# Kernel optimization log

Hardware: AMD Instinct MI355X
Metric: run time of the kernel (lower is better)

## Reference

```python
import jax, jax.numpy as jnp
import numpy as np

# dims
B, L, D, H, HD, V, FF, NL = 1, 1024, 1024, 16, 64, 32000, 2816, 2
THETA = 500000.0
EPS = 1e-5
BOI, EOI = 31998, 31999
NEG = jnp.float32(-1e30)  # stands in for -inf in the additive mask


def setup_inputs() -> dict:
    key = jax.random.key(0)
    ks = jax.random.split(key, 12)
    tokens = jax.random.randint(ks[0], (B, L), 0, 31998)
    # inject two well-formed image spans per sequence (boi .. eoi)
    tokens = tokens.at[:, 100].set(BOI).at[:, 300].set(EOI)
    tokens = tokens.at[:, 500].set(BOI).at[:, 800].set(EOI)
    s = 0.02
    n = lambda k, shape: (jax.random.normal(k, shape, jnp.float32) * s)
    return {
        "tokens": tokens,
        "tok_emb": n(ks[1], (V, D)),
        "wq": n(ks[2], (NL, D, D)),
        "wk": n(ks[3], (NL, D, D)),
        "wv": n(ks[4], (NL, D, D)),
        "wo": n(ks[5], (NL, D, D)),
        "w1": n(ks[6], (NL, FF, D)),
        "w2": n(ks[7], (NL, D, FF)),
        "w3": n(ks[8], (NL, FF, D)),
        "attn_norm_w": jnp.ones((NL, D), jnp.float32),
        "ffn_norm_w": jnp.ones((NL, D), jnp.float32),
        "final_norm_w": jnp.ones((D,), jnp.float32),
        "w_out": n(ks[9], (V, D)),
    }


def rmsnorm(x, w):
    xf = x.astype(jnp.float32)
    y = xf * jax.lax.rsqrt(jnp.mean(xf * xf, axis=-1, keepdims=True) + EPS)
    return y.astype(x.dtype) * w


def rope_cos_sin():
    inv = 1.0 / (THETA ** (jnp.arange(0, HD, 2, dtype=jnp.float32) / HD))  # [HD/2]
    ang = jnp.arange(L, dtype=jnp.float32)[:, None] * inv[None, :]        # [L, HD/2]
    return jnp.cos(ang), jnp.sin(ang)


def apply_rope(x, cos, sin):
    # x: [B, L, H, HD]; pairs (even, odd) rotated by complex freqs_cis
    xr = x.astype(jnp.float32).reshape(B, L, H, HD // 2, 2)
    xe, xo = xr[..., 0], xr[..., 1]
    c = cos[None, :, None, :]
    s = sin[None, :, None, :]
    out = jnp.stack([xe * c - xo * s, xe * s + xo * c], axis=-1).reshape(B, L, H, HD)
    return out.astype(x.dtype)


def transfusion_mask(tokens):
    # causal everywhere + fully bidirectional within each boi..eoi span
    is_boi = tokens == BOI
    is_eoi = tokens == EOI
    boi_cnt = jnp.cumsum(is_boi.astype(jnp.int32), axis=1)          # inclusive
    eoi_before = jnp.cumsum(is_eoi.astype(jnp.int32), axis=1) - is_eoi.astype(jnp.int32)
    in_span = boi_cnt > eoi_before                                   # [B, L]
    same_span = (in_span[:, :, None] & in_span[:, None, :]) & (
        boi_cnt[:, :, None] == boi_cnt[:, None, :]
    )
    causal = jnp.arange(L)[:, None] >= jnp.arange(L)[None, :]        # [L, L]
    allowed = causal[None] | same_span                                # [B, L, L]
    return jnp.where(allowed, jnp.float32(0.0), NEG)


def reference(tokens, tok_emb, wq, wk, wv, wo, w1, w2, w3,
              attn_norm_w, ffn_norm_w, final_norm_w, w_out):
    h = tok_emb[tokens]                                # [B, L, D]
    cos, sin = rope_cos_sin()
    mask = transfusion_mask(tokens)[:, None]           # [B, 1, L, L]
    scale = 1.0 / jnp.sqrt(jnp.float32(HD))
    for l in range(NL):
        xn = rmsnorm(h, attn_norm_w[l])
        q = (xn @ wq[l].T).reshape(B, L, H, HD)
        k = (xn @ wk[l].T).reshape(B, L, H, HD)
        v = (xn @ wv[l].T).reshape(B, L, H, HD)
        q = apply_rope(q, cos, sin)
        k = apply_rope(k, cos, sin)
        q, k, v = (t.transpose(0, 2, 1, 3) for t in (q, k, v))  # [B, H, L, HD]
        scores = jnp.einsum("bhqd,bhkd->bhqk", q, k) * scale + mask
        p = jax.nn.softmax(scores.astype(jnp.float32), axis=-1).astype(q.dtype)
        attn = jnp.einsum("bhqk,bhkd->bhqd", p, v)
        attn = attn.transpose(0, 2, 1, 3).reshape(B, L, D)
        h = h + attn @ wo[l].T
        xn = rmsnorm(h, ffn_norm_w[l])
        h = h + (jax.nn.silu(xn @ w1[l].T) * (xn @ w3[l].T)) @ w2[l].T
    logits = rmsnorm(h, final_norm_w) @ w_out.T        # [B, L, V]
    return logits
```

## Files before the change

kernel.cpp:

```cpp
#include <hip/hip_runtime.h>
#include <hip/hip_bf16.h>
#include <stdint.h>

typedef unsigned short u16;
typedef __bf16 bf16x8 __attribute__((ext_vector_type(8)));
typedef u16 u16x8 __attribute__((ext_vector_type(8)));
typedef float f32x4 __attribute__((ext_vector_type(4)));

#define SEQ   1024
#define DM    1024
#define NHEADS 16
#define HDIM  64
#define VOC   32000
#define FFD   2816
#define NLAY  2

__device__ __forceinline__ u16 f2b(float f) {
    unsigned x = __builtin_bit_cast(unsigned, f);
    unsigned r = x + 0x7fffu + ((x >> 16) & 1u);
    return (u16)(r >> 16);
}
__device__ __forceinline__ float b2f(u16 u) {
    unsigned x = ((unsigned)u) << 16;
    return __builtin_bit_cast(float, x);
}
__device__ __forceinline__ float grpmax16(float v) {
    v = fmaxf(v, __shfl_xor(v, 1)); v = fmaxf(v, __shfl_xor(v, 2));
    v = fmaxf(v, __shfl_xor(v, 4)); v = fmaxf(v, __shfl_xor(v, 8));
    return v;
}
__device__ __forceinline__ float grpsum16(float v) {
    v += __shfl_xor(v, 1); v += __shfl_xor(v, 2);
    v += __shfl_xor(v, 4); v += __shfl_xor(v, 8);
    return v;
}

__device__ __forceinline__ void gll16(const void* g, void* l) {
    __builtin_amdgcn_global_load_lds(
        (__attribute__((address_space(1))) void*)(uintptr_t)g,
        (__attribute__((address_space(3))) void*)(uint32_t)(uintptr_t)l,
        16, 0, 0);
}
template <int N> __device__ __forceinline__ void vwait() {
    if constexpr (N == 0)       asm volatile("s_waitcnt vmcnt(0)" ::: "memory");
    else if constexpr (N == 4)  asm volatile("s_waitcnt vmcnt(4)" ::: "memory");
    else if constexpr (N == 6)  asm volatile("s_waitcnt vmcnt(6)" ::: "memory");
    else if constexpr (N == 8)  asm volatile("s_waitcnt vmcnt(8)" ::: "memory");
    else if constexpr (N == 10) asm volatile("s_waitcnt vmcnt(10)" ::: "memory");
    else if constexpr (N == 16) asm volatile("s_waitcnt vmcnt(16)" ::: "memory");
}
__device__ __forceinline__ int xcd_swz(int bid, int nwg) {
    const int q = nwg >> 3, r = nwg & 7;
    const int xcd = bid & 7, j = bid >> 3;
    const int start = (xcd < r) ? xcd * (q + 1) : r * (q + 1) + (xcd - r) * q;
    return start + j;
}

struct CvtArgs { const float* s[8]; u16* d[8]; int cum[9]; };
__global__ __launch_bounds__(256) void cvt_all_kernel(CvtArgs a) {
    const int stride = gridDim.x * 256;
    const int total = a.cum[8];
    for (int u = blockIdx.x * 256 + threadIdx.x; u < total; u += stride) {
        int g = 0;
#pragma unroll
        for (int k = 1; k < 8; ++k) g += (u >= a.cum[k]) ? 1 : 0;
        const int local = u - a.cum[g];
        const float4* sp = (const float4*)a.s[g] + (size_t)local * 4;
        const float4 x0 = sp[0], x1 = sp[1], x2 = sp[2], x3 = sp[3];
        ushort4 p0, p1, p2, p3;
        p0.x = f2b(x0.x); p0.y = f2b(x0.y); p0.z = f2b(x0.z); p0.w = f2b(x0.w);
        p1.x = f2b(x1.x); p1.y = f2b(x1.y); p1.z = f2b(x1.z); p1.w = f2b(x1.w);
        p2.x = f2b(x2.x); p2.y = f2b(x2.y); p2.z = f2b(x2.z); p2.w = f2b(x2.w);
        p3.x = f2b(x3.x); p3.y = f2b(x3.y); p3.z = f2b(x3.z); p3.w = f2b(x3.w);
        ushort4* dp = (ushort4*)a.d[g] + (size_t)local * 4;
        dp[0] = p0; dp[1] = p1; dp[2] = p2; dp[3] = p3;
    }
}

__global__ __launch_bounds__(256) void embed_kernel(const int* __restrict__ tok,
    const float* __restrict__ emb, float* __restrict__ h) {
    const int l = blockIdx.x;
    const int t = tok[l];
    ((float4*)(h + (size_t)l * DM))[threadIdx.x] =
        ((const float4*)(emb + (size_t)t * DM))[threadIdx.x];
}

__global__ __launch_bounds__(256) void ropetab_kernel(float* __restrict__ cosb,
                                                      float* __restrict__ sinb) {
    const int idx = blockIdx.x * 256 + threadIdx.x;
    const int l = idx >> 5, j = idx & 31;
    const float inv = __expf(-((float)j * (1.0f / 32.0f)) * 13.122363377404328f);
    const float ang = (float)l * inv;
    cosb[idx] = cosf(ang);
    sinb[idx] = sinf(ang);
}

__global__ void span_kernel(const int* __restrict__ tok, int* __restrict__ span,
                            int* __restrict__ tmask) {
    __shared__ int sb[SEQ], se[SEQ];
    __shared__ int tm[SEQ / 64];
    const int t = threadIdx.x;
    const int v = tok[t];
    const int bo = (v == 31998) ? 1 : 0;
    const int eo = (v == 31999) ? 1 : 0;
    sb[t] = bo; se[t] = eo;
    if (t < SEQ / 64) tm[t] = 0;
    __syncthreads();
    for (int o = 1; o < SEQ; o <<= 1) {
        int a = 0, b = 0;
        if (t >= o) { a = sb[t - o]; b = se[t - o]; }
        __syncthreads();
        sb[t] += a; se[t] += b;
        __syncthreads();
    }
    const int bc = sb[t];
    const int ec = se[t] - eo;
    const int id = (bc > ec) ? bc : 0;
    span[t] = id;
    if (id > 0) atomicOr(&tm[t >> 6], 1 << ((id - 1) & 31));
    __syncthreads();
    if (t < SEQ / 64) tmask[t] = tm[t];
}

__global__ __launch_bounds__(256) void rmsnorm_kernel(const float* __restrict__ x,
    const float* __restrict__ w, u16* __restrict__ o) {
    const int row = blockIdx.x;
    const float4 xv = ((const float4*)(x + (size_t)row * DM))[threadIdx.x];
    float ss = xv.x * xv.x + xv.y * xv.y + xv.z * xv.z + xv.w * xv.w;
    for (int off = 32; off; off >>= 1) ss += __shfl_xor(ss, off);
    __shared__ float red[4];
    const int lane = threadIdx.x & 63, wvi = threadIdx.x >> 6;
    if (lane == 0) red[wvi] = ss;
    __syncthreads();
    const float tot = red[0] + red[1] + red[2] + red[3];
    const float sc = rsqrtf(tot * (1.0f / (float)DM) + 1e-5f);
    const float4 wv4 = ((const float4*)w)[threadIdx.x];
    ushort4 ov;
    ov.x = f2b(xv.x * sc * wv4.x);
    ov.y = f2b(xv.y * sc * wv4.y);
    ov.z = f2b(xv.z * sc * wv4.z);
    ov.w = f2b(xv.w * sc * wv4.w);
    ((ushort4*)(o + (size_t)row * DM))[threadIdx.x] = ov;
}

template <int RESID, int BM, int BN>
__global__ __launch_bounds__(256) void gemm_p_kernel(const u16* __restrict__ A,
    const u16* __restrict__ B, float* __restrict__ C, const float* __restrict__ res,
    int N, int K) {
    constexpr int AL = BM / 32, BL = BN / 32, LOADS = AL + BL;
    constexpr int MF = BM / 32, NF = BN / 32;
    __shared__ __align__(16) u16 sA[2][BM * 64];
    __shared__ __align__(16) u16 sB[2][BN * 64];
    const int nwg = gridDim.x * gridDim.y;
    const int lid = xcd_swz(blockIdx.y * gridDim.x + blockIdx.x, nwg);
    const int tm = (lid % gridDim.x) * BM, tn = (lid / gridDim.x) * BN;
    const int tid = threadIdx.x, lane = tid & 63, wid = tid >> 6;
    const int wm = wid >> 1, wn = wid & 1, fr = lane & 15, g = lane >> 4;

    const u16* ap[AL]; const u16* bp[BL];
#pragma unroll
    for (int j = 0; j < AL; ++j) {
        const int idx = j * 256 + tid, r = idx >> 3, gr = (idx & 7) ^ (r & 7);
        ap[j] = A + (size_t)(tm + r) * K + gr * 8;
    }
#pragma unroll
    for (int j = 0; j < BL; ++j) {
        const int idx = j * 256 + tid, r = idx >> 3, gr = (idx & 7) ^ (r & 7);
        bp[j] = B + (size_t)(tn + r) * K + gr * 8;
    }

    f32x4 acc[MF][NF] = {};
    const int NT = K >> 6;
#pragma unroll
    for (int j = 0; j < AL; ++j) gll16(ap[j], &sA[0][(j * 256 + tid) * 8]);
#pragma unroll
    for (int j = 0; j < BL; ++j) gll16(bp[j], &sB[0][(j * 256 + tid) * 8]);

    int p = 0;
    for (int t = 0; t < NT; ++t) {
        if (t + 1 < NT) {
#pragma unroll
            for (int j = 0; j < AL; ++j) gll16(ap[j] + (t + 1) * 64, &sA[p ^ 1][(j * 256 + tid) * 8]);
#pragma unroll
            for (int j = 0; j < BL; ++j) gll16(bp[j] + (t + 1) * 64, &sB[p ^ 1][(j * 256 + tid) * 8]);
            vwait<LOADS>();
        } else {
            vwait<0>();
        }
        __builtin_amdgcn_s_barrier();
        __builtin_amdgcn_sched_barrier(0);
        bf16x8 af[MF][2], bfv[NF][2];
#pragma unroll
        for (int m = 0; m < MF; ++m)
#pragma unroll
            for (int ks = 0; ks < 2; ++ks) {
                const int row = wm * (BM / 2) + m * 16 + fr;
                const int gr = (ks * 4 + g) ^ (row & 7);
                af[m][ks] = *(const bf16x8*)&sA[p][row * 64 + gr * 8];
            }
#pragma unroll
        for (int n = 0; n < NF; ++n)
#pragma unroll
            for (int ks = 0; ks < 2; ++ks) {
                const int row = wn * (BN / 2) + n * 16 + fr;
                const int gr = (ks * 4 + g) ^ (row & 7);
                bfv[n][ks] = *(const bf16x8*)&sB[p][row * 64 + gr * 8];
            }
        __builtin_amdgcn_s_setprio(1);
#pragma unroll
        for (int m = 0; m < MF; ++m)
#pragma unroll
            for (int n = 0; n < NF; ++n)
#pragma unroll
                for (int ks = 0; ks < 2; ++ks)
                    acc[m][n] = __builtin_amdgcn_mfma_f32_16x16x32_bf16(af[m][ks], bfv[n][ks], acc[m][n], 0, 0, 0);
        __builtin_amdgcn_s_setprio(0);
        __builtin_amdgcn_s_barrier();
        p ^= 1;
    }

    const int cr = (lane >> 4) * 4, cc = lane & 15;
#pragma unroll
    for (int m = 0; m < MF; ++m)
#pragma unroll
        for (int n = 0; n < NF; ++n) {
            const int row0 = tm + wm * (BM / 2) + m * 16 + cr;
            const int col = tn + wn * (BN / 2) + n * 16 + cc;
#pragma unroll
            for (int r = 0; r < 4; ++r) {
                const size_t idx = (size_t)(row0 + r) * N + col;
                float v = acc[m][n][r];
                if (RESID) v += res[idx];
                C[idx] = v;
            }
        }
}

template <int RESID>
__global__ __launch_bounds__(512, 2) void gemm_big_kernel(const u16* __restrict__ A,
    const float* __restrict__ B, float* __restrict__ C, const float* __restrict__ res,
    int N, int K) {
    __shared__ __align__(16) u16 sA[2][256 * 64];
    __shared__ __align__(16) u16 sB[2][256 * 64];
    const int nwg = gridDim.x * gridDim.y;
    const int lid = xcd_swz(blockIdx.y * gridDim.x + blockIdx.x, nwg);
    const int tm = (lid % gridDim.x) * 256;
    const int tn = (lid / gridDim.x) * 256;
    const int tid = threadIdx.x, lane = tid & 63, wid = tid >> 6;
    const int wm = wid >> 2, wn = wid & 3;
    const int fr = lane & 15, g = lane >> 4;

    const u16* ap[4];
#pragma unroll
    for (int j = 0; j < 4; ++j) {
        const int idx = j * 512 + tid, r = idx >> 3, gr = (idx & 7) ^ (r & 7);
        ap[j] = A + (size_t)(tm + r) * K + gr * 8;
    }
    const float* bp[4];
    int bst[4];
#pragma unroll
    for (int j = 0; j < 4; ++j) {
        const int G = j * 512 + tid, r = G >> 3, gr = G & 7;
        bp[j] = B + (size_t)(tn + r) * K + gr * 8;
        bst[j] = r * 64 + ((gr ^ (r & 7)) * 8);
    }

    auto cvtst = [&](int b, int j, const float4& x0, const float4& x1) {
        bf16x8 v;
        v[0] = (__bf16)x0.x; v[1] = (__bf16)x0.y; v[2] = (__bf16)x0.z; v[3] = (__bf16)x0.w;
        v[4] = (__bf16)x1.x; v[5] = (__bf16)x1.y; v[6] = (__bf16)x1.z; v[7] = (__bf16)x1.w;
        *(bf16x8*)&sB[b][bst[j]] = v;
    };

    f32x4 acc[8][4] = {};
    const int NT = K >> 6;

    {
#pragma unroll
        for (int j = 0; j < 4; ++j) gll16(ap[j], &sA[0][(j * 512 + tid) * 8]);
        float4 b0 = *(const float4*)(bp[0]), b1 = *(const float4*)(bp[0] + 4);
        float4 b2 = *(const float4*)(bp[1]), b3 = *(const float4*)(bp[1] + 4);
        cvtst(0, 0, b0, b1); cvtst(0, 1, b2, b3);
        b0 = *(const float4*)(bp[2]); b1 = *(const float4*)(bp[2] + 4);
        b2 = *(const float4*)(bp[3]); b3 = *(const float4*)(bp[3] + 4);
        cvtst(0, 2, b0, b1); cvtst(0, 3, b2, b3);
        __syncthreads();
    }

    int p = 0;
    for (int t = 0; t < NT; ++t) {
        const bool pre = (t + 1 < NT);
        float4 b0, b1, b2, b3;
        if (pre) {
#pragma unroll
            for (int j = 0; j < 4; ++j) gll16(ap[j] + (t + 1) * 64, &sA[p ^ 1][(j * 512 + tid) * 8]);
            b0 = *(const float4*)(bp[0] + (t + 1) * 64); b1 = *(const float4*)(bp[0] + (t + 1) * 64 + 4);
            b2 = *(const float4*)(bp[1] + (t + 1) * 64); b3 = *(const float4*)(bp[1] + (t + 1) * 64 + 4);
        }
        bf16x8 bfv[4][2];
#pragma unroll
        for (int mq = 0; mq < 4; ++mq) {
            if (mq == 0) {
#pragma unroll
                for (int n = 0; n < 4; ++n)
#pragma unroll
                    for (int ks = 0; ks < 2; ++ks) {
                        const int row = wn * 64 + n * 16 + fr;
                        const int gr = (ks * 4 + g) ^ (row & 7);
                        bfv[n][ks] = *(const bf16x8*)&sB[p][row * 64 + gr * 8];
                    }
            }
            if (mq == 2 && pre) {
                cvtst(p ^ 1, 0, b0, b1); cvtst(p ^ 1, 1, b2, b3);
                b0 = *(const float4*)(bp[2] + (t + 1) * 64); b1 = *(const float4*)(bp[2] + (t + 1) * 64 + 4);
                b2 = *(const float4*)(bp[3] + (t + 1) * 64); b3 = *(const float4*)(bp[3] + (t + 1) * 64 + 4);
            }
            bf16x8 af[2][2];
#pragma unroll
            for (int i = 0; i < 2; ++i)
#pragma unroll
                for (int ks = 0; ks < 2; ++ks) {
                    const int row = wm * 128 + (mq * 2 + i) * 16 + fr;
                    const int gr = (ks * 4 + g) ^ (row & 7);
                    af[i][ks] = *(const bf16x8*)&sA[p][row * 64 + gr * 8];
                }
            __builtin_amdgcn_s_setprio(1);
#pragma unroll
            for (int i = 0; i < 2; ++i)
#pragma unroll
                for (int n = 0; n < 4; ++n)
#pragma unroll
                    for (int ks = 0; ks < 2; ++ks)
                        acc[mq * 2 + i][n] = __builtin_amdgcn_mfma_f32_16x16x32_bf16(
                            af[i][ks], bfv[n][ks], acc[mq * 2 + i][n], 0, 0, 0);
            __builtin_amdgcn_s_setprio(0);
            if (mq < 3) __builtin_amdgcn_s_barrier();
        }
        if (pre) { cvtst(p ^ 1, 2, b0, b1); cvtst(p ^ 1, 3, b2, b3); }
        __syncthreads();
        p ^= 1;
    }

    const int cr = (lane >> 4) * 4, cc = lane & 15;
#pragma unroll
    for (int m = 0; m < 8; ++m)
#pragma unroll
        for (int n = 0; n < 4; ++n) {
            const int row0 = tm + wm * 128 + m * 16 + cr;
            const int col = tn + wn * 64 + n * 16 + cc;
#pragma unroll
            for (int r = 0; r < 4; ++r) {
                const size_t idx = (size_t)(row0 + r) * N + col;
                float v = acc[m][n][r];
                if (RESID) v += res[idx];
                C[idx] = v;
            }
        }
}

__global__ __launch_bounds__(256) void qkv_kernel(const u16* __restrict__ A,
    const u16* __restrict__ Bq, const u16* __restrict__ Bk, const u16* __restrict__ Bv,
    const float* __restrict__ cosb, const float* __restrict__ sinb,
    u16* __restrict__ qb, u16* __restrict__ kb, u16* __restrict__ vb) {
    __shared__ __align__(16) u16 sA[2][128 * 64];
    __shared__ __align__(16) u16 sB[2][128 * 64];
    const int lid = xcd_swz(blockIdx.y * gridDim.x + blockIdx.x, 8 * 24);
    const int tm = (lid % 8) * 128;
    const int yy = lid / 8;
    const int mat = yy >> 3;
    const int tn = (yy & 7) * 128;
    const u16* B = (mat == 0) ? Bq : (mat == 1) ? Bk : Bv;
    u16* out = (mat == 0) ? qb : (mat == 1) ? kb : vb;
    const int tid = threadIdx.x, lane = tid & 63, wid = tid >> 6;
    const int wm = wid >> 1, wn = wid & 1, fr = lane & 15, g = lane >> 4;

    const u16* ap[4]; const u16* bp[4];
#pragma unroll
    for (int j = 0; j < 4; ++j) {
        const int idx = j * 256 + tid, r = idx >> 3, gr = (idx & 7) ^ (r & 7);
        ap[j] = A + (size_t)(tm + r) * DM + gr * 8;
        bp[j] = B + (size_t)(tn + r) * DM + gr * 8;
    }

    f32x4 acc[4][4] = {};
#pragma unroll
    for (int j = 0; j < 4; ++j) gll16(ap[j], &sA[0][(j * 256 + tid) * 8]);
#pragma unroll
    for (int j = 0; j < 4; ++j) gll16(bp[j], &sB[0][(j * 256 + tid) * 8]);

    int p = 0;
    for (int t = 0; t < DM / 64; ++t) {
        if (t + 1 < DM / 64) {
#pragma unroll
            for (int j = 0; j < 4; ++j) gll16(ap[j] + (t + 1) * 64, &sA[p ^ 1][(j * 256 + tid) * 8]);
#pragma unroll
            for (int j = 0; j < 4; ++j) gll16(bp[j] + (t + 1) * 64, &sB[p ^ 1][(j * 256 + tid) * 8]);
            vwait<8>();
        } else {
            vwait<0>();
        }
        __builtin_amdgcn_s_barrier();
        __builtin_amdgcn_sched_barrier(0);
        bf16x8 af[4][2], bfv[4][2];
#pragma unroll
        for (int m = 0; m < 4; ++m)
#pragma unroll
            for (int ks = 0; ks < 2; ++ks) {
                const int row = wm * 64 + m * 16 + fr;
                const int gr = (ks * 4 + g) ^ (row & 7);
                af[m][ks] = *(const bf16x8*)&sA[p][row * 64 + gr * 8];
            }
#pragma unroll
        for (int n = 0; n < 4; ++n)
#pragma unroll
            for (int ks = 0; ks < 2; ++ks) {
                const int row = wn * 64 + n * 16 + fr;
                const int gr = (ks * 4 + g) ^ (row & 7);
                bfv[n][ks] = *(const bf16x8*)&sB[p][row * 64 + gr * 8];
            }
        __builtin_amdgcn_s_setprio(1);
#pragma unroll
        for (int m = 0; m < 4; ++m)
#pragma unroll
            for (int n = 0; n < 4; ++n)
#pragma unroll
                for (int ks = 0; ks < 2; ++ks)
                    acc[m][n] = __builtin_amdgcn_mfma_f32_16x16x32_bf16(af[m][ks], bfv[n][ks], acc[m][n], 0, 0, 0);
        __builtin_amdgcn_s_setprio(0);
        __builtin_amdgcn_s_barrier();
        p ^= 1;
    }

    const int cr = (lane >> 4) * 4, cc = lane & 15;
    if (mat < 2) {
#pragma unroll
        for (int m = 0; m < 4; ++m)
#pragma unroll
            for (int n = 0; n < 4; ++n) {
                const int row0 = tm + wm * 64 + m * 16 + cr;
                const int col = tn + wn * 64 + n * 16 + cc;
                const int j = (n * 16 + cc) >> 1;
#pragma unroll
                for (int r = 0; r < 4; ++r) {
                    const int row = row0 + r;
                    const float c = cosb[row * 32 + j];
                    const float s = sinb[row * 32 + j];
                    const float v = acc[m][n][r];
                    const float pv = __shfl_xor(v, 1);
                    const float o = (cc & 1) ? (pv * s + v * c) : (v * c - pv * s);
                    out[(size_t)row * DM + col] = f2b(o);
                }
            }
    } else {
#pragma unroll
        for (int m = 0; m < 4; ++m)
#pragma unroll
            for (int n = 0; n < 4; ++n) {
                const int row0 = tm + wm * 64 + m * 16 + cr;
                const int col = tn + wn * 64 + n * 16 + cc;
#pragma unroll
                for (int r = 0; r < 4; ++r)
                    out[(size_t)(row0 + r) * DM + col] = f2b(acc[m][n][r]);
            }
    }
}

__global__ __launch_bounds__(256) void ffn13_kernel(const u16* __restrict__ A,
    const u16* __restrict__ B1, const u16* __restrict__ B3, u16* __restrict__ Z) {
    __shared__ __align__(16) u16 sA[2][128 * 64];
    __shared__ __align__(16) u16 sB1[2][64 * 64];
    __shared__ __align__(16) u16 sB3[2][64 * 64];
    const int lid = xcd_swz(blockIdx.y * gridDim.x + blockIdx.x, 8 * (FFD / 64));
    const int tm = (lid % 8) * 128;
    const int tn = (lid / 8) * 64;
    const int tid = threadIdx.x, lane = tid & 63, wid = tid >> 6;
    const int wm = wid >> 1, wn = wid & 1, fr = lane & 15, g = lane >> 4;

    const u16* ap[4]; const u16* b1p[2]; const u16* b3p[2];
#pragma unroll
    for (int j = 0; j < 4; ++j) {
        const int idx = j * 256 + tid, r = idx >> 3, gr = (idx & 7) ^ (r & 7);
        ap[j] = A + (size_t)(tm + r) * DM + gr * 8;
    }
#pragma unroll
    for (int j = 0; j < 2; ++j) {
        const int idx = j * 256 + tid, r = idx >> 3, gr = (idx & 7) ^ (r & 7);
        b1p[j] = B1 + (size_t)(tn + r) * DM + gr * 8;
        b3p[j] = B3 + (size_t)(tn + r) * DM + gr * 8;
    }

    f32x4 acc1[4][2] = {}, acc3[4][2] = {};
#pragma unroll
    for (int j = 0; j < 4; ++j) gll16(ap[j], &sA[0][(j * 256 + tid) * 8]);
#pragma unroll
    for (int j = 0; j < 2; ++j) gll16(b1p[j], &sB1[0][(j * 256 + tid) * 8]);
#pragma unroll
    for (int j = 0; j < 2; ++j) gll16(b3p[j], &sB3[0][(j * 256 + tid) * 8]);

    int p = 0;
    for (int t = 0; t < DM / 64; ++t) {
        if (t + 1 < DM / 64) {
#pragma unroll
            for (int j = 0; j < 4; ++j) gll16(ap[j] + (t + 1) * 64, &sA[p ^ 1][(j * 256 + tid) * 8]);
#pragma unroll
            for (int j = 0; j < 2; ++j) gll16(b1p[j] + (t + 1) * 64, &sB1[p ^ 1][(j * 256 + tid) * 8]);
#pragma unroll
            for (int j = 0; j < 2; ++j) gll16(b3p[j] + (t + 1) * 64, &sB3[p ^ 1][(j * 256 + tid) * 8]);
            vwait<8>();
        } else {
            vwait<0>();
        }
        __builtin_amdgcn_s_barrier();
        __builtin_amdgcn_sched_barrier(0);
        bf16x8 af[4][2], b1v[2][2], b3v[2][2];
#pragma unroll
        for (int m = 0; m < 4; ++m)
#pragma unroll
            for (int ks = 0; ks < 2; ++ks) {
                const int row = wm * 64 + m * 16 + fr;
                const int gr = (ks * 4 + g) ^ (row & 7);
                af[m][ks] = *(const bf16x8*)&sA[p][row * 64 + gr * 8];
            }
#pragma unroll
        for (int n = 0; n < 2; ++n)
#pragma unroll
            for (int ks = 0; ks < 2; ++ks) {
                const int row = wn * 32 + n * 16 + fr;
                const int gr = (ks * 4 + g) ^ (row & 7);
                b1v[n][ks] = *(const bf16x8*)&sB1[p][row * 64 + gr * 8];
                b3v[n][ks] = *(const bf16x8*)&sB3[p][row * 64 + gr * 8];
            }
        __builtin_amdgcn_s_setprio(1);
#pragma unroll
        for (int m = 0; m < 4; ++m)
#pragma unroll
            for (int n = 0; n < 2; ++n)
#pragma unroll
                for (int ks = 0; ks < 2; ++ks) {
                    acc1[m][n] = __builtin_amdgcn_mfma_f32_16x16x32_bf16(af[m][ks], b1v[n][ks], acc1[m][n], 0, 0, 0);
                    acc3[m][n] = __builtin_amdgcn_mfma_f32_16x16x32_bf16(af[m][ks], b3v[n][ks], acc3[m][n], 0, 0, 0);
                }
        __builtin_amdgcn_s_setprio(0);
        __builtin_amdgcn_s_barrier();
        p ^= 1;
    }

    const int cr = (lane >> 4) * 4, cc = lane & 15;
#pragma unroll
    for (int m = 0; m < 4; ++m)
#pragma unroll
        for (int n = 0; n < 2; ++n) {
            const int row0 = tm + wm * 64 + m * 16 + cr;
            const int col = tn + wn * 32 + n * 16 + cc;
#pragma unroll
            for (int r = 0; r < 4; ++r) {
                const float a1 = acc1[m][n][r];
                const float a3 = acc3[m][n][r];
                const float z = a1 / (1.f + __expf(-a1)) * a3;
                Z[(size_t)(row0 + r) * FFD + col] = f2b(z);
            }
        }
}

__global__ __launch_bounds__(256) void fattn_kernel(const u16* __restrict__ qb,
    const u16* __restrict__ kb, const u16* __restrict__ vb,
    const int* __restrict__ span, const int* __restrict__ tmask, u16* __restrict__ ob) {
    __shared__ __align__(16) u16 sK[64][72];
    __shared__ __align__(16) u16 sVT[64][72];
    __shared__ __align__(16) u16 sP[4][16][72];
    const int tid = threadIdx.x, lane = tid & 63, wq = tid >> 6;
    const int g = lane >> 4, fr = lane & 15;
    const int head = blockIdx.y;
    const int qbase = blockIdx.x * 64;
    const int qmask = tmask[blockIdx.x];

    bf16x8 qfr[2];
    {
        const u16* qp = qb + (size_t)(qbase + wq * 16 + fr) * DM + head * HDIM + g * 8;
        qfr[0] = *(const bf16x8*)(qp);
        qfr[1] = *(const bf16x8*)(qp + 32);
    }
    int sq[4];
#pragma unroll
    for (int r = 0; r < 4; ++r) sq[r] = span[qbase + wq * 16 + g * 4 + r];

    float m_old[4] = {-1e30f, -1e30f, -1e30f, -1e30f};
    float lsum[4] = {0.f, 0.f, 0.f, 0.f};
    f32x4 acc[4] = {};

    for (int kt = 0; kt < SEQ / 64; ++kt) {
        const int kb0 = kt * 64;
        if (kb0 > qbase && (qmask & tmask[kt]) == 0) continue;
        __syncthreads();
        {
            const int r = tid >> 2, c0 = (tid & 3) * 16;
            const u16* src = kb + (size_t)(kb0 + r) * DM + head * HDIM + c0;
            *(u16x8*)&sK[r][c0]     = *(const u16x8*)(src);
            *(u16x8*)&sK[r][c0 + 8] = *(const u16x8*)(src + 8);
        }
        {
            const int k = tid & 63, d0 = (tid >> 6) * 16;
            const u16* src = vb + (size_t)(kb0 + k) * DM + head * HDIM + d0;
            const u16x8 v0 = *(const u16x8*)(src);
            const u16x8 v1 = *(const u16x8*)(src + 8);
#pragma unroll
            for (int j = 0; j < 8; ++j) {
                sVT[d0 + j][k]     = v0[j];
                sVT[d0 + 8 + j][k] = v1[j];
            }
        }
        __syncthreads();

        f32x4 accs[4] = {};
        __builtin_amdgcn_s_setprio(1);
#pragma unroll
        for (int nf = 0; nf < 4; ++nf)
#pragma unroll
            for (int kf = 0; kf < 2; ++kf) {
                const bf16x8 kfv = *(const bf16x8*)&sK[nf * 16 + fr][g * 8 + kf * 32];
                accs[nf] = __builtin_amdgcn_mfma_f32_16x16x32_bf16(qfr[kf], kfv, accs[nf], 0, 0, 0);
            }
        __builtin_amdgcn_s_setprio(0);

        float sv[4][4]; bool al[4][4];
        if (kb0 + 63 <= qbase) {
#pragma unroll
            for (int nf = 0; nf < 4; ++nf)
#pragma unroll
                for (int r = 0; r < 4; ++r) {
                    al[nf][r] = true;
                    sv[nf][r] = accs[nf][r] * 0.125f;
                }
        } else {
            int spk[4];
#pragma unroll
            for (int nf = 0; nf < 4; ++nf) spk[nf] = span[kb0 + nf * 16 + fr];
#pragma unroll
            for (int nf = 0; nf < 4; ++nf) {
                const int key = kb0 + nf * 16 + fr;
#pragma unroll
                for (int r = 0; r < 4; ++r) {
                    const int q = qbase + wq * 16 + g * 4 + r;
                    al[nf][r] = (key <= q) || (sq[r] > 0 && spk[nf] == sq[r]);
                    sv[nf][r] = al[nf][r] ? accs[nf][r] * 0.125f : -1e30f;
                }
            }
        }
        float alpha[4], ls[4];
#pragma unroll
        for (int r = 0; r < 4; ++r) {
            float mn = fmaxf(fmaxf(sv[0][r], sv[1][r]), fmaxf(sv[2][r], sv[3][r]));
            mn = grpmax16(mn);
            const float mnew = fmaxf(m_old[r], mn);
            alpha[r] = __expf(m_old[r] - mnew);
            m_old[r] = mnew;
            ls[r] = 0.f;
        }
        u16 pb[4][4];
#pragma unroll
        for (int nf = 0; nf < 4; ++nf)
#pragma unroll
            for (int r = 0; r < 4; ++r) {
                const float p = al[nf][r] ? __expf(sv[nf][r] - m_old[r]) : 0.f;
                ls[r] += p;
                pb[nf][r] = f2b(p);
            }
#pragma unroll
        for (int r = 0; r < 4; ++r) {
            lsum[r] = lsum[r] * alpha[r] + grpsum16(ls[r]);
#pragma unroll
            for (int nf = 0; nf < 4; ++nf) acc[nf][r] *= alpha[r];
        }
#pragma unroll
        for (int nf = 0; nf < 4; ++nf)
#pragma unroll
            for (int r = 0; r < 4; ++r)
                sP[wq][g * 4 + r][nf * 16 + fr] = pb[nf][r];

        __builtin_amdgcn_s_setprio(1);
#pragma unroll
        for (int nf = 0; nf < 4; ++nf)
#pragma unroll
            for (int kf = 0; kf < 2; ++kf) {
                const bf16x8 pa  = *(const bf16x8*)&sP[wq][fr][g * 8 + kf * 32];
                const bf16x8 vtb = *(const bf16x8*)&sVT[nf * 16 + fr][g * 8 + kf * 32];
                acc[nf] = __builtin_amdgcn_mfma_f32_16x16x32_bf16(pa, vtb, acc[nf], 0, 0, 0);
            }
        __builtin_amdgcn_s_setprio(0);
    }

#pragma unroll
    for (int nf = 0; nf < 4; ++nf)
#pragma unroll
        for (int r = 0; r < 4; ++r) {
            const int q = qbase + wq * 16 + g * 4 + r;
            const int d = nf * 16 + fr;
            ob[(size_t)q * DM + head * HDIM + d] = f2b(acc[nf][r] / lsum[r]);
        }
}

extern "C" void kernel_launch(void* const* d_in, const int* in_sizes, int n_in,
                              void* d_out, int out_size, void* d_ws, size_t ws_size,
                              hipStream_t stream) {
    (void)in_sizes; (void)n_in; (void)out_size; (void)ws_size;
    const int*   tokens   = (const int*)d_in[0];
    const float* tok_emb  = (const float*)d_in[1];
    const float* wq       = (const float*)d_in[2];
    const float* wk       = (const float*)d_in[3];
    const float* wvw      = (const float*)d_in[4];
    const float* wo       = (const float*)d_in[5];
    const float* w1       = (const float*)d_in[6];
    const float* w2       = (const float*)d_in[7];
    const float* w3       = (const float*)d_in[8];
    const float* attn_nw  = (const float*)d_in[9];
    const float* ffn_nw   = (const float*)d_in[10];
    const float* final_nw = (const float*)d_in[11];
    const float* w_out    = (const float*)d_in[12];
    float* logits = (float*)d_out;

    char* ws = (char*)d_ws;
    size_t off = 0;
    auto alloc = [&](size_t b) { size_t o = off; off += (b + 255) & ~(size_t)255; return o; };
    float* h    = (float*)(ws + alloc((size_t)SEQ * DM * 4));
    u16*   xn   = (u16*)  (ws + alloc((size_t)SEQ * DM * 2));
    u16*   qb   = (u16*)  (ws + alloc((size_t)SEQ * DM * 2));
    u16*   kb   = (u16*)  (ws + alloc((size_t)SEQ * DM * 2));
    u16*   vb   = (u16*)  (ws + alloc((size_t)SEQ * DM * 2));
    u16*   ab   = (u16*)  (ws + alloc((size_t)SEQ * DM * 2));
    u16*   zb   = (u16*)  (ws + alloc((size_t)SEQ * FFD * 2));
    float* cosb = (float*)(ws + alloc((size_t)SEQ * 32 * 4));
    float* sinb = (float*)(ws + alloc((size_t)SEQ * 32 * 4));
    int*   span = (int*)  (ws + alloc((size_t)SEQ * 4));
    int*   tmask= (int*)  (ws + alloc((size_t)(SEQ / 64) * 4));
    const size_t nQ = (size_t)NLAY * DM * DM;
    const size_t nF = (size_t)NLAY * FFD * DM;
    u16* wqb = (u16*)(ws + alloc(nQ * 2));
    u16* wkb = (u16*)(ws + alloc(nQ * 2));
    u16* wvb = (u16*)(ws + alloc(nQ * 2));
    u16* wob = (u16*)(ws + alloc(nQ * 2));
    u16* w1b = (u16*)(ws + alloc(nF * 2));
    u16* w2b = (u16*)(ws + alloc(nF * 2));
    u16* w3b = (u16*)(ws + alloc(nF * 2));

    CvtArgs ca;
    const float* srcs[7] = {wq, wk, wvw, wo, w1, w2, w3};
    u16* dsts[7] = {wqb, wkb, wvb, wob, w1b, w2b, w3b};
    const size_t cnts[7] = {nQ, nQ, nQ, nQ, nF, nF, nF};
    int cum = 0;
    for (int i = 0; i < 7; ++i) {
        ca.s[i] = srcs[i]; ca.d[i] = dsts[i]; ca.cum[i] = cum;
        cum += (int)(cnts[i] / 16);
    }
    ca.s[7] = wq; ca.d[7] = wqb;
    ca.cum[7] = cum; ca.cum[8] = cum;
    cvt_all_kernel<<<2048, 256, 0, stream>>>(ca);

    embed_kernel<<<SEQ, 256, 0, stream>>>(tokens, tok_emb, h);
    ropetab_kernel<<<(SEQ * 32) / 256, 256, 0, stream>>>(cosb, sinb);
    span_kernel<<<1, SEQ, 0, stream>>>(tokens, span, tmask);

    for (int l = 0; l < NLAY; ++l) {
        rmsnorm_kernel<<<SEQ, 256, 0, stream>>>(h, attn_nw + (size_t)l * DM, xn);
        qkv_kernel<<<dim3(8, 24), 256, 0, stream>>>(
            xn, wqb + (size_t)l * DM * DM, wkb + (size_t)l * DM * DM, wvb + (size_t)l * DM * DM,
            cosb, sinb, qb, kb, vb);
        fattn_kernel<<<dim3(SEQ / 64, NHEADS), 256, 0, stream>>>(qb, kb, vb, span, tmask, ab);
        gemm_p_kernel<1, 128, 64><<<dim3(8, 16), 256, 0, stream>>>(
            ab, wob + (size_t)l * DM * DM, h, h, DM, DM);

        rmsnorm_kernel<<<SEQ, 256, 0, stream>>>(h, ffn_nw + (size_t)l * DM, xn);
        ffn13_kernel<<<dim3(8, FFD / 64), 256, 0, stream>>>(
            xn, w1b + (size_t)l * FFD * DM, w3b + (size_t)l * FFD * DM, zb);
        gemm_p_kernel<1, 128, 64><<<dim3(8, 16), 256, 0, stream>>>(
            zb, w2b + (size_t)l * DM * FFD, h, h, DM, FFD);
    }

    rmsnorm_kernel<<<SEQ, 256, 0, stream>>>(h, final_nw, xn);
    gemm_big_kernel<0><<<dim3(SEQ / 256, VOC / 256), 512, 0, stream>>>(
        xn, w_out, logits, nullptr, VOC, DM);
}
```

Baseline: 356.7 us.

## Fuse fp32-to-bf16 weight conversion into GEMM B-tile loads

```diff
diff --git a/kernel.cpp b/kernel.cpp
--- a/kernel.cpp
+++ b/kernel.cpp
@@ -43,11 +43,12 @@
 }
 template <int N> __device__ __forceinline__ void vwait() {
     if constexpr (N == 0)       asm volatile("s_waitcnt vmcnt(0)" ::: "memory");
-    else if constexpr (N == 4)  asm volatile("s_waitcnt vmcnt(4)" ::: "memory");
-    else if constexpr (N == 6)  asm volatile("s_waitcnt vmcnt(6)" ::: "memory");
     else if constexpr (N == 8)  asm volatile("s_waitcnt vmcnt(8)" ::: "memory");
-    else if constexpr (N == 10) asm volatile("s_waitcnt vmcnt(10)" ::: "memory");
-    else if constexpr (N == 16) asm volatile("s_waitcnt vmcnt(16)" ::: "memory");
+    else if constexpr (N == 12) asm volatile("s_waitcnt vmcnt(12)" ::: "memory");
+}
+__device__ __forceinline__ void lgkm_barrier() {
+    asm volatile("s_waitcnt lgkmcnt(0)" ::: "memory");
+    __builtin_amdgcn_s_barrier();
 }
 __device__ __forceinline__ int xcd_swz(int bid, int nwg) {
     const int q = nwg >> 3, r = nwg & 7;
@@ -55,26 +56,11 @@
     const int start = (xcd < r) ? xcd * (q + 1) : r * (q + 1) + (xcd - r) * q;
     return start + j;
 }
-
-struct CvtArgs { const float* s[8]; u16* d[8]; int cum[9]; };
-__global__ __launch_bounds__(256) void cvt_all_kernel(CvtArgs a) {
-    const int stride = gridDim.x * 256;
-    const int total = a.cum[8];
-    for (int u = blockIdx.x * 256 + threadIdx.x; u < total; u += stride) {
-        int g = 0;
-#pragma unroll
-        for (int k = 1; k < 8; ++k) g += (u >= a.cum[k]) ? 1 : 0;
-        const int local = u - a.cum[g];
-        const float4* sp = (const float4*)a.s[g] + (size_t)local * 4;
-        const float4 x0 = sp[0], x1 = sp[1], x2 = sp[2], x3 = sp[3];
-        ushort4 p0, p1, p2, p3;
-        p0.x = f2b(x0.x); p0.y = f2b(x0.y); p0.z = f2b(x0.z); p0.w = f2b(x0.w);
-        p1.x = f2b(x1.x); p1.y = f2b(x1.y); p1.z = f2b(x1.z); p1.w = f2b(x1.w);
-        p2.x = f2b(x2.x); p2.y = f2b(x2.y); p2.z = f2b(x2.z); p2.w = f2b(x2.w);
-        p3.x = f2b(x3.x); p3.y = f2b(x3.y); p3.z = f2b(x3.z); p3.w = f2b(x3.w);
-        ushort4* dp = (ushort4*)a.d[g] + (size_t)local * 4;
-        dp[0] = p0; dp[1] = p1; dp[2] = p2; dp[3] = p3;
-    }
+__device__ __forceinline__ void cvt_store(u16* dst, const float4& x0, const float4& x1) {
+    bf16x8 v;
+    v[0] = (__bf16)x0.x; v[1] = (__bf16)x0.y; v[2] = (__bf16)x0.z; v[3] = (__bf16)x0.w;
+    v[4] = (__bf16)x1.x; v[5] = (__bf16)x1.y; v[6] = (__bf16)x1.z; v[7] = (__bf16)x1.w;
+    *(bf16x8*)dst = v;
 }
 
 __global__ __launch_bounds__(256) void embed_kernel(const int* __restrict__ tok,
@@ -143,11 +129,13 @@
     ((ushort4*)(o + (size_t)row * DM))[threadIdx.x] = ov;
 }
 
+
 template <int RESID, int BM, int BN>
 __global__ __launch_bounds__(256) void gemm_p_kernel(const u16* __restrict__ A,
-    const u16* __restrict__ B, float* __restrict__ C, const float* __restrict__ res,
+    const float* __restrict__ B, float* __restrict__ C, const float* __restrict__ res,
     int N, int K) {
-    constexpr int AL = BM / 32, BL = BN / 32, LOADS = AL + BL;
+    constexpr int AL = BM / 32;
+    constexpr int GB = BN / 32;
     constexpr int MF = BM / 32, NF = BN / 32;
     __shared__ __align__(16) u16 sA[2][BM * 64];
     __shared__ __align__(16) u16 sB[2][BN * 64];
@@ -157,33 +145,47 @@
     const int tid = threadIdx.x, lane = tid & 63, wid = tid >> 6;
     const int wm = wid >> 1, wn = wid & 1, fr = lane & 15, g = lane >> 4;
 
-    const u16* ap[AL]; const u16* bp[BL];
+    const u16* ap[AL];
 #pragma unroll
     for (int j = 0; j < AL; ++j) {
         const int idx = j * 256 + tid, r = idx >> 3, gr = (idx & 7) ^ (r & 7);
         ap[j] = A + (size_t)(tm + r) * K + gr * 8;
     }
-#pragma unroll
-    for (int j = 0; j < BL; ++j) {
-        const int idx = j * 256 + tid, r = idx >> 3, gr = (idx & 7) ^ (r & 7);
+    const float* bp[GB]; int bst[GB];
+#pragma unroll
+    for (int j = 0; j < GB; ++j) {
+        const int G = j * 256 + tid, r = G >> 3, gr = G & 7;
         bp[j] = B + (size_t)(tn + r) * K + gr * 8;
+        bst[j] = r * 64 + ((gr ^ (r & 7)) * 8);
     }
 
     f32x4 acc[MF][NF] = {};
     const int NT = K >> 6;
-#pragma unroll
-    for (int j = 0; j < AL; ++j) gll16(ap[j], &sA[0][(j * 256 + tid) * 8]);
-#pragma unroll
-    for (int j = 0; j < BL; ++j) gll16(bp[j], &sB[0][(j * 256 + tid) * 8]);
+    {
+#pragma unroll
+        for (int j = 0; j < AL; ++j) gll16(ap[j], &sA[0][(j * 256 + tid) * 8]);
+#pragma unroll
+        for (int j = 0; j < GB; ++j) {
+            const float4 x0 = *(const float4*)(bp[j]);
+            const float4 x1 = *(const float4*)(bp[j] + 4);
+            cvt_store(&sB[0][bst[j]], x0, x1);
+        }
+        __syncthreads();
+    }
 
     int p = 0;
     for (int t = 0; t < NT; ++t) {
-        if (t + 1 < NT) {
+        const bool pre = (t + 1 < NT);
+        float4 xb[GB][2];
+        if (pre) {
 #pragma unroll
             for (int j = 0; j < AL; ++j) gll16(ap[j] + (t + 1) * 64, &sA[p ^ 1][(j * 256 + tid) * 8]);
 #pragma unroll
-            for (int j = 0; j < BL; ++j) gll16(bp[j] + (t + 1) * 64, &sB[p ^ 1][(j * 256 + tid) * 8]);
-            vwait<LOADS>();
+            for (int j = 0; j < GB; ++j) {
+                xb[j][0] = *(const float4*)(bp[j] + (t + 1) * 64);
+                xb[j][1] = *(const float4*)(bp[j] + (t + 1) * 64 + 4);
+            }
+            vwait<AL + 2 * GB>();
         } else {
             vwait<0>();
         }
@@ -215,7 +217,11 @@
                 for (int ks = 0; ks < 2; ++ks)
                     acc[m][n] = __builtin_amdgcn_mfma_f32_16x16x32_bf16(af[m][ks], bfv[n][ks], acc[m][n], 0, 0, 0);
         __builtin_amdgcn_s_setprio(0);
-        __builtin_amdgcn_s_barrier();
+        if (pre) {
+#pragma unroll
+            for (int j = 0; j < GB; ++j) cvt_store(&sB[p ^ 1][bst[j]], xb[j][0], xb[j][1]);
+        }
+        lgkm_barrier();
         p ^= 1;
     }
 
@@ -266,10 +272,7 @@
     }
 
     auto cvtst = [&](int b, int j, const float4& x0, const float4& x1) {
-        bf16x8 v;
-        v[0] = (__bf16)x0.x; v[1] = (__bf16)x0.y; v[2] = (__bf16)x0.z; v[3] = (__bf16)x0.w;
-        v[4] = (__bf16)x1.x; v[5] = (__bf16)x1.y; v[6] = (__bf16)x1.z; v[7] = (__bf16)x1.w;
-        *(bf16x8*)&sB[b][bst[j]] = v;
+        cvt_store(&sB[b][bst[j]], x0, x1);
     };
 
     f32x4 acc[8][4] = {};
@@ -359,7 +362,7 @@
 }
 
 __global__ __launch_bounds__(256) void qkv_kernel(const u16* __restrict__ A,
-    const u16* __restrict__ Bq, const u16* __restrict__ Bk, const u16* __restrict__ Bv,
+    const float* __restrict__ Bq, const float* __restrict__ Bk, const float* __restrict__ Bv,
     const float* __restrict__ cosb, const float* __restrict__ sinb,
     u16* __restrict__ qb, u16* __restrict__ kb, u16* __restrict__ vb) {
     __shared__ __align__(16) u16 sA[2][128 * 64];
@@ -369,33 +372,51 @@
     const int yy = lid / 8;
     const int mat = yy >> 3;
     const int tn = (yy & 7) * 128;
-    const u16* B = (mat == 0) ? Bq : (mat == 1) ? Bk : Bv;
+    const float* B = (mat == 0) ? Bq : (mat == 1) ? Bk : Bv;
     u16* out = (mat == 0) ? qb : (mat == 1) ? kb : vb;
     const int tid = threadIdx.x, lane = tid & 63, wid = tid >> 6;
     const int wm = wid >> 1, wn = wid & 1, fr = lane & 15, g = lane >> 4;
 
-    const u16* ap[4]; const u16* bp[4];
+    const u16* ap[4];
 #pragma unroll
     for (int j = 0; j < 4; ++j) {
         const int idx = j * 256 + tid, r = idx >> 3, gr = (idx & 7) ^ (r & 7);
         ap[j] = A + (size_t)(tm + r) * DM + gr * 8;
+    }
+    const float* bp[4]; int bst[4];
+#pragma unroll
+    for (int j = 0; j < 4; ++j) {
+        const int G = j * 256 + tid, r = G >> 3, gr = G & 7;
         bp[j] = B + (size_t)(tn + r) * DM + gr * 8;
+        bst[j] = r * 64 + ((gr ^ (r & 7)) * 8);
     }
 
     f32x4 acc[4][4] = {};
-#pragma unroll
-    for (int j = 0; j < 4; ++j) gll16(ap[j], &sA[0][(j * 256 + tid) * 8]);
-#pragma unroll
-    for (int j = 0; j < 4; ++j) gll16(bp[j], &sB[0][(j * 256 + tid) * 8]);
+    {
+#pragma unroll
+        for (int j = 0; j < 4; ++j) gll16(ap[j], &sA[0][(j * 256 + tid) * 8]);
+#pragma unroll
+        for (int j = 0; j < 4; ++j) {
+            const float4 x0 = *(const float4*)(bp[j]);
+            const float4 x1 = *(const float4*)(bp[j] + 4);
+            cvt_store(&sB[0][bst[j]], x0, x1);
+        }
+        __syncthreads();
+    }
 
     int p = 0;
     for (int t = 0; t < DM / 64; ++t) {
-        if (t + 1 < DM / 64) {
+        const bool pre = (t + 1 < DM / 64);
+        float4 xb[4][2];
+        if (pre) {
 #pragma unroll
             for (int j = 0; j < 4; ++j) gll16(ap[j] + (t + 1) * 64, &sA[p ^ 1][(j * 256 + tid) * 8]);
 #pragma unroll
-            for (int j = 0; j < 4; ++j) gll16(bp[j] + (t + 1) * 64, &sB[p ^ 1][(j * 256 + tid) * 8]);
-            vwait<8>();
+            for (int j = 0; j < 4; ++j) {
+                xb[j][0] = *(const float4*)(bp[j] + (t + 1) * 64);
+                xb[j][1] = *(const float4*)(bp[j] + (t + 1) * 64 + 4);
+            }
+            vwait<12>();
         } else {
             vwait<0>();
         }
@@ -427,7 +448,11 @@
                 for (int ks = 0; ks < 2; ++ks)
                     acc[m][n] = __builtin_amdgcn_mfma_f32_16x16x32_bf16(af[m][ks], bfv[n][ks], acc[m][n], 0, 0, 0);
         __builtin_amdgcn_s_setprio(0);
-        __builtin_amdgcn_s_barrier();
+        if (pre) {
+#pragma unroll
+            for (int j = 0; j < 4; ++j) cvt_store(&sB[p ^ 1][bst[j]], xb[j][0], xb[j][1]);
+        }
+        lgkm_barrier();
         p ^= 1;
     }
 
@@ -466,7 +491,7 @@
 }
 
 __global__ __launch_bounds__(256) void ffn13_kernel(const u16* __restrict__ A,
-    const u16* __restrict__ B1, const u16* __restrict__ B3, u16* __restrict__ Z) {
+    const float* __restrict__ B1, const float* __restrict__ B3, u16* __restrict__ Z) {
     __shared__ __align__(16) u16 sA[2][128 * 64];
     __shared__ __align__(16) u16 sB1[2][64 * 64];
     __shared__ __align__(16) u16 sB3[2][64 * 64];
@@ -476,37 +501,52 @@
     const int tid = threadIdx.x, lane = tid & 63, wid = tid >> 6;
     const int wm = wid >> 1, wn = wid & 1, fr = lane & 15, g = lane >> 4;
 
-    const u16* ap[4]; const u16* b1p[2]; const u16* b3p[2];
+    const u16* ap[4];
 #pragma unroll
     for (int j = 0; j < 4; ++j) {
         const int idx = j * 256 + tid, r = idx >> 3, gr = (idx & 7) ^ (r & 7);
         ap[j] = A + (size_t)(tm + r) * DM + gr * 8;
     }
+    const float* b1p[2]; const float* b3p[2]; int bst[2];
 #pragma unroll
     for (int j = 0; j < 2; ++j) {
-        const int idx = j * 256 + tid, r = idx >> 3, gr = (idx & 7) ^ (r & 7);
+        const int G = j * 256 + tid, r = G >> 3, gr = G & 7;
         b1p[j] = B1 + (size_t)(tn + r) * DM + gr * 8;
         b3p[j] = B3 + (size_t)(tn + r) * DM + gr * 8;
+        bst[j] = r * 64 + ((gr ^ (r & 7)) * 8);
     }
 
     f32x4 acc1[4][2] = {}, acc3[4][2] = {};
-#pragma unroll
-    for (int j = 0; j < 4; ++j) gll16(ap[j], &sA[0][(j * 256 + tid) * 8]);
-#pragma unroll
-    for (int j = 0; j < 2; ++j) gll16(b1p[j], &sB1[0][(j * 256 + tid) * 8]);
-#pragma unroll
-    for (int j = 0; j < 2; ++j) gll16(b3p[j], &sB3[0][(j * 256 + tid) * 8]);
+    {
+#pragma unroll
+        for (int j = 0; j < 4; ++j) gll16(ap[j], &sA[0][(j * 256 + tid) * 8]);
+#pragma unroll
+        for (int j = 0; j < 2; ++j) {
+            float4 x0 = *(const float4*)(b1p[j]);
+            float4 x1 = *(const float4*)(b1p[j] + 4);
+            cvt_store(&sB1[0][bst[j]], x0, x1);
+            x0 = *(const float4*)(b3p[j]);
+            x1 = *(const float4*)(b3p[j] + 4);
+            cvt_store(&sB3[0][bst[j]], x0, x1);
+        }
+        __syncthreads();
+    }
 
     int p = 0;
     for (int t = 0; t < DM / 64; ++t) {
-        if (t + 1 < DM / 64) {
+        const bool pre = (t + 1 < DM / 64);
+        float4 x1b[2][2], x3b[2][2];
+        if (pre) {
 #pragma unroll
             for (int j = 0; j < 4; ++j) gll16(ap[j] + (t + 1) * 64, &sA[p ^ 1][(j * 256 + tid) * 8]);
 #pragma unroll
-            for (int j = 0; j < 2; ++j) gll16(b1p[j] + (t + 1) * 64, &sB1[p ^ 1][(j * 256 + tid) * 8]);
-#pragma unroll
-            for (int j = 0; j < 2; ++j) gll16(b3p[j] + (t + 1) * 64, &sB3[p ^ 1][(j * 256 + tid) * 8]);
-            vwait<8>();
+            for (int j = 0; j < 2; ++j) {
+                x1b[j][0] = *(const float4*)(b1p[j] + (t + 1) * 64);
+                x1b[j][1] = *(const float4*)(b1p[j] + (t + 1) * 64 + 4);
+                x3b[j][0] = *(const float4*)(b3p[j] + (t + 1) * 64);
+                x3b[j][1] = *(const float4*)(b3p[j] + (t + 1) * 64 + 4);
+            }
+            vwait<12>();
         } else {
             vwait<0>();
         }
@@ -541,7 +581,14 @@
                     acc3[m][n] = __builtin_amdgcn_mfma_f32_16x16x32_bf16(af[m][ks], b3v[n][ks], acc3[m][n], 0, 0, 0);
                 }
         __builtin_amdgcn_s_setprio(0);
-        __builtin_amdgcn_s_barrier();
+        if (pre) {
+#pragma unroll
+            for (int j = 0; j < 2; ++j) {
+                cvt_store(&sB1[p ^ 1][bst[j]], x1b[j][0], x1b[j][1]);
+                cvt_store(&sB3[p ^ 1][bst[j]], x3b[j][0], x3b[j][1]);
+            }
+        }
+        lgkm_barrier();
         p ^= 1;
     }
 
@@ -732,28 +779,6 @@
     float* sinb = (float*)(ws + alloc((size_t)SEQ * 32 * 4));
     int*   span = (int*)  (ws + alloc((size_t)SEQ * 4));
     int*   tmask= (int*)  (ws + alloc((size_t)(SEQ / 64) * 4));
-    const size_t nQ = (size_t)NLAY * DM * DM;
-    const size_t nF = (size_t)NLAY * FFD * DM;
-    u16* wqb = (u16*)(ws + alloc(nQ * 2));
-    u16* wkb = (u16*)(ws + alloc(nQ * 2));
-    u16* wvb = (u16*)(ws + alloc(nQ * 2));
-    u16* wob = (u16*)(ws + alloc(nQ * 2));
-    u16* w1b = (u16*)(ws + alloc(nF * 2));
-    u16* w2b = (u16*)(ws + alloc(nF * 2));
-    u16* w3b = (u16*)(ws + alloc(nF * 2));
-
-    CvtArgs ca;
-    const float* srcs[7] = {wq, wk, wvw, wo, w1, w2, w3};
-    u16* dsts[7] = {wqb, wkb, wvb, wob, w1b, w2b, w3b};
-    const size_t cnts[7] = {nQ, nQ, nQ, nQ, nF, nF, nF};
-    int cum = 0;
-    for (int i = 0; i < 7; ++i) {
-        ca.s[i] = srcs[i]; ca.d[i] = dsts[i]; ca.cum[i] = cum;
-        cum += (int)(cnts[i] / 16);
-    }
-    ca.s[7] = wq; ca.d[7] = wqb;
-    ca.cum[7] = cum; ca.cum[8] = cum;
-    cvt_all_kernel<<<2048, 256, 0, stream>>>(ca);
 
     embed_kernel<<<SEQ, 256, 0, stream>>>(tokens, tok_emb, h);
     ropetab_kernel<<<(SEQ * 32) / 256, 256, 0, stream>>>(cosb, sinb);
@@ -762,17 +787,17 @@
     for (int l = 0; l < NLAY; ++l) {
         rmsnorm_kernel<<<SEQ, 256, 0, stream>>>(h, attn_nw + (size_t)l * DM, xn);
         qkv_kernel<<<dim3(8, 24), 256, 0, stream>>>(
-            xn, wqb + (size_t)l * DM * DM, wkb + (size_t)l * DM * DM, wvb + (size_t)l * DM * DM,
+            xn, wq + (size_t)l * DM * DM, wk + (size_t)l * DM * DM, wvw + (size_t)l * DM * DM,
             cosb, sinb, qb, kb, vb);
         fattn_kernel<<<dim3(SEQ / 64, NHEADS), 256, 0, stream>>>(qb, kb, vb, span, tmask, ab);
         gemm_p_kernel<1, 128, 64><<<dim3(8, 16), 256, 0, stream>>>(
-            ab, wob + (size_t)l * DM * DM, h, h, DM, DM);
+            ab, wo + (size_t)l * DM * DM, h, h, DM, DM);
 
         rmsnorm_kernel<<<SEQ, 256, 0, stream>>>(h, ffn_nw + (size_t)l * DM, xn);
         ffn13_kernel<<<dim3(8, FFD / 64), 256, 0, stream>>>(
-            xn, w1b + (size_t)l * FFD * DM, w3b + (size_t)l * FFD * DM, zb);
+            xn, w1 + (size_t)l * FFD * DM, w3 + (size_t)l * FFD * DM, zb);
         gemm_p_kernel<1, 128, 64><<<dim3(8, 16), 256, 0, stream>>>(
-            zb, w2b + (size_t)l * DM * FFD, h, h, DM, FFD);
+            zb, w2 + (size_t)l * DM * FFD, h, h, DM, FFD);
     }
 
     rmsnorm_kernel<<<SEQ, 256, 0, stream>>>(h, final_nw, xn);
```

New measurement: 543.3 us. +52.3%, slower.

## Prefetch fp32 B-operand halves two K-tiles ahead with fine-grained vmcnt waits

Applied to the files above, without the earlier changes.

```diff
diff --git a/kernel.cpp b/kernel.cpp
--- a/kernel.cpp
+++ b/kernel.cpp
@@ -275,27 +275,38 @@
     f32x4 acc[8][4] = {};
     const int NT = K >> 6;
 
+    float4 h1[4], h2[4];
+
     {
-#pragma unroll
-        for (int j = 0; j < 4; ++j) gll16(ap[j], &sA[0][(j * 512 + tid) * 8]);
         float4 b0 = *(const float4*)(bp[0]), b1 = *(const float4*)(bp[0] + 4);
         float4 b2 = *(const float4*)(bp[1]), b3 = *(const float4*)(bp[1] + 4);
+        float4 b4 = *(const float4*)(bp[2]), b5 = *(const float4*)(bp[2] + 4);
+        float4 b6 = *(const float4*)(bp[3]), b7 = *(const float4*)(bp[3] + 4);
+#pragma unroll
+        for (int j = 0; j < 4; ++j) gll16(ap[j], &sA[0][(j * 512 + tid) * 8]);
         cvtst(0, 0, b0, b1); cvtst(0, 1, b2, b3);
-        b0 = *(const float4*)(bp[2]); b1 = *(const float4*)(bp[2] + 4);
-        b2 = *(const float4*)(bp[3]); b3 = *(const float4*)(bp[3] + 4);
-        cvtst(0, 2, b0, b1); cvtst(0, 3, b2, b3);
-        __syncthreads();
+        cvtst(0, 2, b4, b5); cvtst(0, 3, b6, b7);
+        if (NT > 1) {
+            h1[0] = *(const float4*)(bp[0] + 64); h1[1] = *(const float4*)(bp[0] + 64 + 4);
+            h1[2] = *(const float4*)(bp[1] + 64); h1[3] = *(const float4*)(bp[1] + 64 + 4);
+            vwait<4>();
+        } else {
+            vwait<0>();
+        }
+        asm volatile("s_waitcnt lgkmcnt(0)" ::: "memory");
+        __builtin_amdgcn_s_barrier();
+        __builtin_amdgcn_sched_barrier(0);
     }
 
     int p = 0;
     for (int t = 0; t < NT; ++t) {
-        const bool pre = (t + 1 < NT);
-        float4 b0, b1, b2, b3;
-        if (pre) {
+        const bool pre1 = (t + 1 < NT);
+        const bool pre2 = (t + 2 < NT);
+        if (pre1) {
 #pragma unroll
             for (int j = 0; j < 4; ++j) gll16(ap[j] + (t + 1) * 64, &sA[p ^ 1][(j * 512 + tid) * 8]);
-            b0 = *(const float4*)(bp[0] + (t + 1) * 64); b1 = *(const float4*)(bp[0] + (t + 1) * 64 + 4);
-            b2 = *(const float4*)(bp[1] + (t + 1) * 64); b3 = *(const float4*)(bp[1] + (t + 1) * 64 + 4);
+            h2[0] = *(const float4*)(bp[2] + (t + 1) * 64); h2[1] = *(const float4*)(bp[2] + (t + 1) * 64 + 4);
+            h2[2] = *(const float4*)(bp[3] + (t + 1) * 64); h2[3] = *(const float4*)(bp[3] + (t + 1) * 64 + 4);
         }
         bf16x8 bfv[4][2];
 #pragma unroll
@@ -310,10 +321,12 @@
                         bfv[n][ks] = *(const bf16x8*)&sB[p][row * 64 + gr * 8];
                     }
             }
-            if (mq == 2 && pre) {
-                cvtst(p ^ 1, 0, b0, b1); cvtst(p ^ 1, 1, b2, b3);
-                b0 = *(const float4*)(bp[2] + (t + 1) * 64); b1 = *(const float4*)(bp[2] + (t + 1) * 64 + 4);
-                b2 = *(const float4*)(bp[3] + (t + 1) * 64); b3 = *(const float4*)(bp[3] + (t + 1) * 64 + 4);
+            if (mq == 2 && pre1) {
+                cvtst(p ^ 1, 0, h1[0], h1[1]); cvtst(p ^ 1, 1, h1[2], h1[3]);
+            }
+            if (mq == 3 && pre2) {
+                h1[0] = *(const float4*)(bp[0] + (t + 2) * 64); h1[1] = *(const float4*)(bp[0] + (t + 2) * 64 + 4);
+                h1[2] = *(const float4*)(bp[1] + (t + 2) * 64); h1[3] = *(const float4*)(bp[1] + (t + 2) * 64 + 4);
             }
             bf16x8 af[2][2];
 #pragma unroll
@@ -336,8 +349,11 @@
             __builtin_amdgcn_s_setprio(0);
             if (mq < 3) __builtin_amdgcn_s_barrier();
         }
-        if (pre) { cvtst(p ^ 1, 2, b0, b1); cvtst(p ^ 1, 3, b2, b3); }
-        __syncthreads();
+        if (pre1) { cvtst(p ^ 1, 2, h2[0], h2[1]); cvtst(p ^ 1, 3, h2[2], h2[3]); }
+        asm volatile("s_waitcnt lgkmcnt(0)" ::: "memory");
+        if (pre2) vwait<4>(); else vwait<0>();
+        __builtin_amdgcn_s_barrier();
+        __builtin_amdgcn_sched_barrier(0);
         p ^= 1;
     }
 
```

Measured after the change: 373.0 us. 1.05x slower.
